# Optimization experiments

Hardware: AMD Instinct MI355X
Metric: run time of the kernel (lower is better)

Reference implementation:

```python
import jax, jax.numpy as jnp
import numpy as np

N_USERS = 100_000
N_ITEMS = 100_000
D = 64
B = 16_384
L_U = 50   # items per user history
N_F = 32   # friends per user
L_I = 50   # users per item history


def setup_inputs() -> dict:
    key = jax.random.key(0)
    ks = jax.random.split(key, 22)
    s = 0.1  # xavier-ish scale for D=64
    return {
        "user_ids": jax.random.randint(ks[0], (B,), 0, N_USERS),
        "item_ids": jax.random.randint(ks[1], (B,), 0, N_ITEMS),
        "user_hist_items": jax.random.randint(ks[2], (B, L_U), 0, N_ITEMS),
        "user_hist_ratings": jax.random.uniform(ks[3], (B, L_U), jnp.float32, 1.0, 5.0),
        "user_friends": jax.random.randint(ks[4], (B, N_F), 0, N_USERS),
        "item_hist_users": jax.random.randint(ks[5], (B, L_I), 0, N_USERS),
        "item_hist_ratings": jax.random.uniform(ks[6], (B, L_I), jnp.float32, 1.0, 5.0),
        "embed_user": jax.random.normal(ks[7], (N_USERS, D), jnp.float32) * s,
        "embed_item": jax.random.normal(ks[8], (N_ITEMS, D), jnp.float32) * s,
        "W1": jax.random.normal(ks[9], (D, D), jnp.float32) * s,
        "W2": jax.random.normal(ks[10], (D, D), jnp.float32) * s,
        "W3": jax.random.normal(ks[11], (D, 1), jnp.float32) * s,
        "W4": jax.random.normal(ks[12], (D, D), jnp.float32) * s,
        "W5": jax.random.normal(ks[13], (D, D), jnp.float32) * s,
        "W6": jax.random.normal(ks[14], (D, 1), jnp.float32) * s,
        "W7": jax.random.normal(ks[15], (D, D), jnp.float32) * s,
        "W8": jax.random.normal(ks[16], (D, D), jnp.float32) * s,
        "W9": jax.random.normal(ks[17], (D, 1), jnp.float32) * s,
        "fc1_w": jax.random.normal(ks[18], (2 * D, D), jnp.float32) * s,
        "fc1_b": jnp.zeros((D,), jnp.float32),
        "fc2_w": jax.random.normal(ks[19], (D, 1), jnp.float32) * s,
        "fc2_b": jnp.zeros((1,), jnp.float32),
    }


def _attention(q_emb, neigh, Wq, Wk, Wa, ratings=None):
    # q_emb: [B, D]; neigh: [B, L, D]; ratings: [B, L] or None
    a = q_emb @ Wq  # [B, D]
    a = a[:, None, :] + neigh @ Wk  # [B, L, D]
    if ratings is not None:
        a = a + ratings[..., None] * neigh
    w = jax.nn.softmax((a @ Wa)[..., 0], axis=1)  # [B, L]
    return jnp.einsum("bl,bld->bd", w, neigh)


def reference(user_ids, item_ids, user_hist_items, user_hist_ratings,
              user_friends, item_hist_users, item_hist_ratings,
              embed_user, embed_item,
              W1, W2, W3, W4, W5, W6, W7, W8, W9,
              fc1_w, fc1_b, fc2_w, fc2_b):
    user_emb = embed_user[user_ids]          # [B, D]
    item_emb = embed_item[item_ids]          # [B, D]

    # user <- rated items attention (W1, W2, W3)
    hist_item_embs = embed_item[user_hist_items]        # [B, L_U, D]
    user_items_emb = _attention(user_emb, hist_item_embs, W1, W2, W3,
                                user_hist_ratings)

    # user <- friends attention (W4, W5, W6)
    friend_embs = embed_user[user_friends]               # [B, N_F, D]
    user_social_emb = _attention(user_emb, friend_embs, W4, W5, W6)

    user_emb_final = user_emb + user_items_emb + user_social_emb

    # item <- interacting users attention (W7, W8, W9)
    hist_user_embs = embed_user[item_hist_users]         # [B, L_I, D]
    item_users_emb = _attention(item_emb, hist_user_embs, W7, W8, W9,
                                item_hist_ratings)
    item_emb_final = item_emb + item_users_emb

    concat = jnp.concatenate([user_emb_final, item_emb_final], axis=1)  # [B, 2D]
    h = jax.nn.relu(concat @ fc1_w + fc1_b)
    out = (h @ fc2_w + fc2_b)[:, 0]  # [B]
    return out
```

## Files before the change

### kernel.cpp

```cpp
#include <hip/hip_runtime.h>
#include <math.h>

#define B_TOTAL 16384
#define D 64
#define L_U 50
#define N_F 32
#define L_I 50

#define PART_OFF 0
#define SUA_OFF  520
#define SWA_OFF  584
#define SUB_OFF  648
#define SUC_OFF  712
#define SWC_OFF  776
#define WAVE_FL  848

__global__ void graphrec_setup(const float* __restrict__ W1, const float* __restrict__ W2,
                               const float* __restrict__ W3, const float* __restrict__ W4,
                               const float* __restrict__ W5, const float* __restrict__ W6,
                               const float* __restrict__ W7, const float* __restrict__ W8,
                               const float* __restrict__ W9, float* __restrict__ u) {
    int t = threadIdx.x;
    int w = t >> 6;
    int d = t & 63;
    const float* Wm;
    const float* Wv;
    switch (w) {
        case 0: Wm = W1; Wv = W3; break;
        case 1: Wm = W2; Wv = W3; break;
        case 2: Wm = W4; Wv = W6; break;
        case 3: Wm = W5; Wv = W6; break;
        case 4: Wm = W7; Wv = W9; break;
        default: Wm = W8; Wv = W9; break;
    }
    float s = 0.f;
    #pragma unroll
    for (int j = 0; j < D; ++j) s = fmaf(Wm[d * D + j], Wv[j], s);
    u[w * D + d] = s;
}

__device__ __forceinline__ float wred_sum(float x) {
    float t;
    #define STEP_ADD(ctrl, rmask)                                                        \
        t = __int_as_float(__builtin_amdgcn_update_dpp(0, __float_as_int(x),             \
                                                       ctrl, rmask, 0xf, false));        \
        x = x + t;
    STEP_ADD(0x111, 0xf)
    STEP_ADD(0x112, 0xf)
    STEP_ADD(0x114, 0xf)
    STEP_ADD(0x118, 0xf)
    STEP_ADD(0x142, 0xa)
    STEP_ADD(0x143, 0xc)
    #undef STEP_ADD
    return __int_as_float(__builtin_amdgcn_readlane(__float_as_int(x), 63));
}
__device__ __forceinline__ float wred_max(float x) {
    const int NEG_INF = 0xFF800000;
    float t;
    #define STEP_MAX(ctrl, rmask)                                                        \
        t = __int_as_float(__builtin_amdgcn_update_dpp(NEG_INF, __float_as_int(x),       \
                                                       ctrl, rmask, 0xf, false));        \
        x = fmaxf(x, t);
    STEP_MAX(0x111, 0xf)
    STEP_MAX(0x112, 0xf)
    STEP_MAX(0x114, 0xf)
    STEP_MAX(0x118, 0xf)
    STEP_MAX(0x142, 0xa)
    STEP_MAX(0x143, 0xc)
    #undef STEP_MAX
    return __int_as_float(__builtin_amdgcn_readlane(__float_as_int(x), 63));
}

__device__ __forceinline__ float segred8(float x) {
    float t;
    t = __int_as_float(__builtin_amdgcn_update_dpp(0, __float_as_int(x), 0x111, 0xf, 0xf, false));
    x = x + t;
    t = __int_as_float(__builtin_amdgcn_update_dpp(0, __float_as_int(x), 0x112, 0xf, 0xf, false));
    x = x + t;
    t = __int_as_float(__builtin_amdgcn_update_dpp(0, __float_as_int(x), 0x114, 0xf, 0xf, false));
    x = x + t;
    return x;
}

template <int L, int NG>
__device__ __forceinline__ void stage8(const float* __restrict__ table,
                                       int idxreg, int sub, int co, float4* buf) {
    #pragma unroll
    for (int g = 0; g < NG; ++g) {
        int r = 8 * g + sub;
        if (r > L - 1) r = L - 1;
        int ridx = __builtin_amdgcn_ds_bpermute(r << 2, idxreg);
        const float* p = table + (unsigned)((ridx << 6) + co);
        buf[2 * g]     = *(const float4*)(p);
        buf[2 * g + 1] = *(const float4*)(p + 4);
    }
}

template <int L, int NG, bool HAS_R>
__device__ __forceinline__ float attn8(float cq, const float* __restrict__ u2,
                                       const float* __restrict__ wa, float r,
                                       int lane, int sub, int cc,
                                       const float4* buf, float* __restrict__ su,
                                       float* __restrict__ sw,
                                       float* __restrict__ part) {
    const float4 uu0 = ((const float4*)u2)[2 * cc];
    const float4 uu1 = ((const float4*)u2)[2 * cc + 1];
    float4 ww0 = {0.f, 0.f, 0.f, 0.f}, ww1 = {0.f, 0.f, 0.f, 0.f};
    if (HAS_R) {
        ww0 = ((const float4*)wa)[2 * cc];
        ww1 = ((const float4*)wa)[2 * cc + 1];
    }

    #pragma unroll
    for (int g = 0; g < NG; ++g) {
        const float4 n0 = buf[2 * g];
        const float4 n1 = buf[2 * g + 1];
        float du = fmaf(n0.x, uu0.x, fmaf(n0.y, uu0.y, fmaf(n0.z, uu0.z,
                   fmaf(n0.w, uu0.w, fmaf(n1.x, uu1.x, fmaf(n1.y, uu1.y,
                   fmaf(n1.z, uu1.z, n1.w * uu1.w)))))));
        du = segred8(du);
        if (HAS_R) {
            float dw = fmaf(n0.x, ww0.x, fmaf(n0.y, ww0.y, fmaf(n0.z, ww0.z,
                       fmaf(n0.w, ww0.w, fmaf(n1.x, ww1.x, fmaf(n1.y, ww1.y,
                       fmaf(n1.z, ww1.z, n1.w * ww1.w)))))));
            dw = segred8(dw);
            if (cc == 7) { su[8 * g + sub] = du; sw[8 * g + sub] = dw; }
        } else {
            if (cc == 7) su[8 * g + sub] = du;
        }
    }

    float sc = cq + su[lane];
    if (HAS_R) sc = fmaf(r, sw[lane], sc);
    sc = (lane < L) ? sc : -1e30f;
    const float m = wred_max(sc);
    const float e = __expf(sc - m);
    const float s = wred_sum(e);
    const float w = e * (1.0f / s);

    float4 a0 = {0.f, 0.f, 0.f, 0.f}, a1 = {0.f, 0.f, 0.f, 0.f};
    #pragma unroll
    for (int g = 0; g < NG; ++g) {
        const float wv = __int_as_float(
            __builtin_amdgcn_ds_bpermute((8 * g + sub) << 2, __float_as_int(w)));
        const float4 n0 = buf[2 * g];
        const float4 n1 = buf[2 * g + 1];
        a0.x = fmaf(wv, n0.x, a0.x); a0.y = fmaf(wv, n0.y, a0.y);
        a0.z = fmaf(wv, n0.z, a0.z); a0.w = fmaf(wv, n0.w, a0.w);
        a1.x = fmaf(wv, n1.x, a1.x); a1.y = fmaf(wv, n1.y, a1.y);
        a1.z = fmaf(wv, n1.z, a1.z); a1.w = fmaf(wv, n1.w, a1.w);
    }

    const int s4 = lane & 4;
    const int pw = lane << 3;
    *(float4*)(part + pw + s4)       = a0;
    *(float4*)(part + pw + (4 ^ s4)) = a1;
    const int rb = (lane & 56) + ((lane & 7) ^ ((lane >> 3) & 4));
    float acc = 0.f;
    #pragma unroll
    for (int s2 = 0; s2 < 8; ++s2) acc += part[rb + 64 * s2];
    return acc;
}

__global__ __launch_bounds__(256, 4) void graphrec_fwd(
        const int* __restrict__ user_ids, const int* __restrict__ item_ids,
        const int* __restrict__ uh_items, const float* __restrict__ uh_rat,
        const int* __restrict__ ufriends,
        const int* __restrict__ ih_users, const float* __restrict__ ih_rat,
        const float* __restrict__ eu, const float* __restrict__ ei,
        const float* __restrict__ W3, const float* __restrict__ W6,
        const float* __restrict__ W9,
        const float* __restrict__ fc1w, const float* __restrict__ fc1b,
        const float* __restrict__ fc2w, const float* __restrict__ fc2b,
        const float* __restrict__ u, float* __restrict__ out) {
    __shared__ __align__(16) float smem[4 * WAVE_FL];
    const int lane = threadIdx.x & 63;
    const int wv = threadIdx.x >> 6;
    const int b = blockIdx.x * 4 + wv;
    float* ws = smem + wv * WAVE_FL;
    const int sub = lane >> 3;
    const int cc  = lane & 7;
    const int co  = cc << 3;

    int idxA = 0, idxB = 0, idxC = 0;
    float rA = 0.f, rC = 0.f;
    if (lane < L_U) {
        idxA = uh_items[b * L_U + lane];
        rA   = uh_rat[b * L_U + lane];
        idxC = ih_users[b * L_I + lane];
        rC   = ih_rat[b * L_I + lane];
    }
    if (lane < N_F) idxB = ufriends[b * N_F + lane];

    float4 bufA[14];
    float4 bufB[8];
    stage8<L_U, 7>(ei, idxA, sub, co, bufA);
    stage8<N_F, 4>(eu, idxB, sub, co, bufB);

    const int uid = user_ids[b];
    const int iid = item_ids[b];
    const float qu = eu[(size_t)uid * D + lane];
    const float qi = ei[(size_t)iid * D + lane];

    const float cqa = wred_sum(qu * u[lane]);
    const float cqb = wred_sum(qu * u[128 + lane]);
    const float cqc = wred_sum(qi * u[256 + lane]);

    const float accA = attn8<L_U, 7, true >(cqa, u + 64, W3, rA, lane, sub, cc,
                                            bufA, ws + SUA_OFF, ws + SWA_OFF,
                                            ws + PART_OFF);
    float4 bufC[14];
    stage8<L_I, 7>(eu, idxC, sub, co, bufC);

    const float accB = attn8<N_F, 4, false>(cqb, u + 192, W6, 0.f, lane, sub, cc,
                                            bufB, ws + SUB_OFF, ws + SUB_OFF,
                                            ws + PART_OFF);
    const float accC = attn8<L_I, 7, true >(cqc, u + 320, W9, rC, lane, sub, cc,
                                            bufC, ws + SUC_OFF, ws + SWC_OFF,
                                            ws + PART_OFF);

    const float uf  = qu + accA + accB;
    const float itf = qi + accC;

    float h0 = fc1b[lane], h1 = 0.f, h2 = 0.f, h3 = 0.f;
    #pragma unroll
    for (int k = 0; k < D; k += 4) {
        h0 = fmaf(__int_as_float(__builtin_amdgcn_readlane(__float_as_int(uf), k + 0)),
                  fc1w[(k + 0) * D + lane], h0);
        h1 = fmaf(__int_as_float(__builtin_amdgcn_readlane(__float_as_int(uf), k + 1)),
                  fc1w[(k + 1) * D + lane], h1);
        h2 = fmaf(__int_as_float(__builtin_amdgcn_readlane(__float_as_int(uf), k + 2)),
                  fc1w[(k + 2) * D + lane], h2);
        h3 = fmaf(__int_as_float(__builtin_amdgcn_readlane(__float_as_int(uf), k + 3)),
                  fc1w[(k + 3) * D + lane], h3);
    }
    #pragma unroll
    for (int k = 0; k < D; k += 4) {
        h0 = fmaf(__int_as_float(__builtin_amdgcn_readlane(__float_as_int(itf), k + 0)),
                  fc1w[(D + k + 0) * D + lane], h0);
        h1 = fmaf(__int_as_float(__builtin_amdgcn_readlane(__float_as_int(itf), k + 1)),
                  fc1w[(D + k + 1) * D + lane], h1);
        h2 = fmaf(__int_as_float(__builtin_amdgcn_readlane(__float_as_int(itf), k + 2)),
                  fc1w[(D + k + 2) * D + lane], h2);
        h3 = fmaf(__int_as_float(__builtin_amdgcn_readlane(__float_as_int(itf), k + 3)),
                  fc1w[(D + k + 3) * D + lane], h3);
    }
    const float h = fmaxf((h0 + h1) + (h2 + h3), 0.f);
    const float o = wred_sum(h * fc2w[lane]);
    if (lane == 0) out[b] = o + fc2b[0];
}

extern "C" void kernel_launch(void* const* d_in, const int* in_sizes, int n_in,
                              void* d_out, int out_size, void* d_ws, size_t ws_size,
                              hipStream_t stream) {
    const int*   user_ids = (const int*)d_in[0];
    const int*   item_ids = (const int*)d_in[1];
    const int*   uh_items = (const int*)d_in[2];
    const float* uh_rat   = (const float*)d_in[3];
    const int*   ufriends = (const int*)d_in[4];
    const int*   ih_users = (const int*)d_in[5];
    const float* ih_rat   = (const float*)d_in[6];
    const float* eu       = (const float*)d_in[7];
    const float* ei       = (const float*)d_in[8];
    const float* W1 = (const float*)d_in[9];
    const float* W2 = (const float*)d_in[10];
    const float* W3 = (const float*)d_in[11];
    const float* W4 = (const float*)d_in[12];
    const float* W5 = (const float*)d_in[13];
    const float* W6 = (const float*)d_in[14];
    const float* W7 = (const float*)d_in[15];
    const float* W8 = (const float*)d_in[16];
    const float* W9 = (const float*)d_in[17];
    const float* fc1w = (const float*)d_in[18];
    const float* fc1b = (const float*)d_in[19];
    const float* fc2w = (const float*)d_in[20];
    const float* fc2b = (const float*)d_in[21];
    float* out = (float*)d_out;
    float* u   = (float*)d_ws;

    graphrec_setup<<<1, 384, 0, stream>>>(W1, W2, W3, W4, W5, W6, W7, W8, W9, u);
    graphrec_fwd<<<B_TOTAL / 4, 256, 0, stream>>>(
        user_ids, item_ids, uh_items, uh_rat, ufriends, ih_users, ih_rat,
        eu, ei, W3, W6, W9, fc1w, fc1b, fc2w, fc2b, u, out);
}
```

Before: 209.0 us.

## Stream neighbor embeddings instead of register-staging, re-gather in weighted-sum pass

Drops the register buffers that prefetched all neighbor rows for each attention before use. Each attention now gathers the rows on the fly for the score pass and gathers them a second time for the weighted-sum pass, with an asm barrier that keeps the compiler from hoisting or merging the reloads. The launch-bounds occupancy hint is removed so the compiler is no longer held to that register budget. The intent is to cut register pressure and raise occupancy, at the cost of twice the gather traffic (the second pass will probably hit L2) and losing the overlap where attention C's loads were issued during attention A.

```diff
diff --git a/kernel.cpp b/kernel.cpp
--- a/kernel.cpp
+++ b/kernel.cpp
@@ -82,27 +82,18 @@
     return x;
 }
 
-template <int L, int NG>
-__device__ __forceinline__ void stage8(const float* __restrict__ table,
-                                       int idxreg, int sub, int co, float4* buf) {
-    #pragma unroll
-    for (int g = 0; g < NG; ++g) {
-        int r = 8 * g + sub;
-        if (r > L - 1) r = L - 1;
-        int ridx = __builtin_amdgcn_ds_bpermute(r << 2, idxreg);
-        const float* p = table + (unsigned)((ridx << 6) + co);
-        buf[2 * g]     = *(const float4*)(p);
-        buf[2 * g + 1] = *(const float4*)(p + 4);
-    }
+__device__ __forceinline__ float dot8(float4 n0, float4 n1, float4 u0, float4 u1) {
+    return fmaf(n0.x, u0.x, fmaf(n0.y, u0.y, fmaf(n0.z, u0.z, fmaf(n0.w, u0.w,
+           fmaf(n1.x, u1.x, fmaf(n1.y, u1.y, fmaf(n1.z, u1.z, n1.w * u1.w)))))));
 }
 
 template <int L, int NG, bool HAS_R>
-__device__ __forceinline__ float attn8(float cq, const float* __restrict__ u2,
-                                       const float* __restrict__ wa, float r,
-                                       int lane, int sub, int cc,
-                                       const float4* buf, float* __restrict__ su,
-                                       float* __restrict__ sw,
-                                       float* __restrict__ part) {
+__device__ __forceinline__ float attn_stream(float cq, const float* __restrict__ u2,
+                                             const float* __restrict__ wa, float r,
+                                             int lane, int sub, int cc, int co,
+                                             const float* __restrict__ table, int idxreg,
+                                             float* __restrict__ su, float* __restrict__ sw,
+                                             float* __restrict__ part) {
     const float4 uu0 = ((const float4*)u2)[2 * cc];
     const float4 uu1 = ((const float4*)u2)[2 * cc + 1];
     float4 ww0 = {0.f, 0.f, 0.f, 0.f}, ww1 = {0.f, 0.f, 0.f, 0.f};
@@ -113,17 +104,15 @@
 
     #pragma unroll
     for (int g = 0; g < NG; ++g) {
-        const float4 n0 = buf[2 * g];
-        const float4 n1 = buf[2 * g + 1];
-        float du = fmaf(n0.x, uu0.x, fmaf(n0.y, uu0.y, fmaf(n0.z, uu0.z,
-                   fmaf(n0.w, uu0.w, fmaf(n1.x, uu1.x, fmaf(n1.y, uu1.y,
-                   fmaf(n1.z, uu1.z, n1.w * uu1.w)))))));
-        du = segred8(du);
+        int rr = 8 * g + sub;
+        if (rr > L - 1) rr = L - 1;
+        int ridx = __builtin_amdgcn_ds_bpermute(rr << 2, idxreg);
+        const float* p = table + (unsigned)((ridx << 6) + co);
+        const float4 n0 = ((const float4*)p)[0];
+        const float4 n1 = ((const float4*)p)[1];
+        float du = segred8(dot8(n0, n1, uu0, uu1));
         if (HAS_R) {
-            float dw = fmaf(n0.x, ww0.x, fmaf(n0.y, ww0.y, fmaf(n0.z, ww0.z,
-                       fmaf(n0.w, ww0.w, fmaf(n1.x, ww1.x, fmaf(n1.y, ww1.y,
-                       fmaf(n1.z, ww1.z, n1.w * ww1.w)))))));
-            dw = segred8(dw);
+            float dw = segred8(dot8(n0, n1, ww0, ww1));
             if (cc == 7) { su[8 * g + sub] = du; sw[8 * g + sub] = dw; }
         } else {
             if (cc == 7) su[8 * g + sub] = du;
@@ -141,10 +130,15 @@
     float4 a0 = {0.f, 0.f, 0.f, 0.f}, a1 = {0.f, 0.f, 0.f, 0.f};
     #pragma unroll
     for (int g = 0; g < NG; ++g) {
+        const int slot = 8 * g + sub;
+        int rr = (slot > L - 1) ? (L - 1) : slot;
+        int ridx = __builtin_amdgcn_ds_bpermute(rr << 2, idxreg);
+        asm volatile("" : "+v"(ridx));
+        const float* p = table + (unsigned)((ridx << 6) + co);
+        const float4 n0 = ((const float4*)p)[0];
+        const float4 n1 = ((const float4*)p)[1];
         const float wv = __int_as_float(
-            __builtin_amdgcn_ds_bpermute((8 * g + sub) << 2, __float_as_int(w)));
-        const float4 n0 = buf[2 * g];
-        const float4 n1 = buf[2 * g + 1];
+            __builtin_amdgcn_ds_bpermute(slot << 2, __float_as_int(w)));
         a0.x = fmaf(wv, n0.x, a0.x); a0.y = fmaf(wv, n0.y, a0.y);
         a0.z = fmaf(wv, n0.z, a0.z); a0.w = fmaf(wv, n0.w, a0.w);
         a1.x = fmaf(wv, n1.x, a1.x); a1.y = fmaf(wv, n1.y, a1.y);
@@ -162,7 +156,7 @@
     return acc;
 }
 
-__global__ __launch_bounds__(256, 4) void graphrec_fwd(
+__global__ __launch_bounds__(256) void graphrec_fwd(
         const int* __restrict__ user_ids, const int* __restrict__ item_ids,
         const int* __restrict__ uh_items, const float* __restrict__ uh_rat,
         const int* __restrict__ ufriends,
@@ -192,11 +186,6 @@
     }
     if (lane < N_F) idxB = ufriends[b * N_F + lane];
 
-    float4 bufA[14];
-    float4 bufB[8];
-    stage8<L_U, 7>(ei, idxA, sub, co, bufA);
-    stage8<N_F, 4>(eu, idxB, sub, co, bufB);
-
     const int uid = user_ids[b];
     const int iid = item_ids[b];
     const float qu = eu[(size_t)uid * D + lane];
@@ -206,18 +195,15 @@
     const float cqb = wred_sum(qu * u[128 + lane]);
     const float cqc = wred_sum(qi * u[256 + lane]);
 
-    const float accA = attn8<L_U, 7, true >(cqa, u + 64, W3, rA, lane, sub, cc,
-                                            bufA, ws + SUA_OFF, ws + SWA_OFF,
-                                            ws + PART_OFF);
-    float4 bufC[14];
-    stage8<L_I, 7>(eu, idxC, sub, co, bufC);
-
-    const float accB = attn8<N_F, 4, false>(cqb, u + 192, W6, 0.f, lane, sub, cc,
-                                            bufB, ws + SUB_OFF, ws + SUB_OFF,
-                                            ws + PART_OFF);
-    const float accC = attn8<L_I, 7, true >(cqc, u + 320, W9, rC, lane, sub, cc,
-                                            bufC, ws + SUC_OFF, ws + SWC_OFF,
-                                            ws + PART_OFF);
+    const float accA = attn_stream<L_U, 7, true >(cqa, u + 64, W3, rA, lane, sub, cc, co,
+                                                  ei, idxA, ws + SUA_OFF, ws + SWA_OFF,
+                                                  ws + PART_OFF);
+    const float accB = attn_stream<N_F, 4, false>(cqb, u + 192, W6, 0.f, lane, sub, cc, co,
+                                                  eu, idxB, ws + SUB_OFF, ws + SUB_OFF,
+                                                  ws + PART_OFF);
+    const float accC = attn_stream<L_I, 7, true >(cqc, u + 320, W9, rC, lane, sub, cc, co,
+                                                  eu, idxC, ws + SUC_OFF, ws + SWC_OFF,
+                                                  ws + PART_OFF);
 
     const float uf  = qu + accA + accB;
     const float itf = qi + accC;
```

New measurement: 239.9 us. +14.8%, slower.
